# Performance work log

Measured on AMD Instinct MI355X. Metric: run time of the kernel, lower is better.

Reference implementation:

```python
import jax, jax.numpy as jnp
import numpy as np

BS, N, H = 8, 64, 512
L = 5
HH, WW = 14, 14


def setup_inputs() -> dict:
    key = jax.random.key(0)
    ks = jax.random.split(key, 6)
    roi_feature_single = jax.random.normal(ks[0], (BS, N, H), dtype=jnp.float32)
    img_featmap = jax.random.normal(ks[1], (BS, H, HH, WW), dtype=jnp.float32)
    # torch init: weight ~ N(0, 0.01), bias = 0
    node_W = jax.random.normal(ks[2], (L, H, H), dtype=jnp.float32) * 0.01
    node_b = jnp.zeros((L, H), dtype=jnp.float32)
    edge_W = jax.random.normal(ks[3], (L, H, H), dtype=jnp.float32) * 0.01
    edge_b = jnp.zeros((L, H), dtype=jnp.float32)
    full_mask = jax.random.randint(ks[4], (BS, N, N), 0, 2, dtype=jnp.int32)
    return {
        "roi_feature_single": roi_feature_single,
        "img_featmap": img_featmap,
        "node_W": node_W,
        "node_b": node_b,
        "edge_W": edge_W,
        "edge_b": edge_b,
        "full_mask": full_mask,
    }


def reference(roi_feature_single, img_featmap, node_W, node_b, edge_W, edge_b, full_mask):
    # mask: [bs, N, N, 1], float
    mask = full_mask.astype(jnp.float32)[..., None]
    denom = jnp.sum(mask, axis=-2) + 1.0  # [bs, N, 1]

    # AdaptiveAvgPool2d((1,1)) on N*N repeats of img_featmap == global mean over (H, W)
    edge_init = jnp.mean(img_featmap, axis=(2, 3))  # [bs, hidden]
    edge_state = jnp.broadcast_to(edge_init[:, None, None, :], (BS, N, N, H))

    node_state = roi_feature_single  # [bs, N, hidden]

    for t in range(L):
        nm = jnp.einsum('bnh,oh->bno', node_state, node_W[t]) + node_b[t]          # node_fc
        em = jnp.einsum('bijh,oh->bijo', edge_state, edge_W[t]) + edge_b[t]        # edge_fc
        col = nm[:, None, :, :]                      # feature_col_large [bs,1,N,h]
        edge_feat = nm[:, :, None, :] + col + em     # row + col + edge messages
        edge_state = jax.nn.leaky_relu(edge_feat)    # negative_slope=0.01 (torch default)
        agg = jnp.sum(edge_state * col * mask, axis=-2)   # masked sum over j -> [bs,N,h]
        node_feat = (nm + agg) / denom
        node_state = node_state + jax.nn.leaky_relu(node_feat)

    roi_col = jnp.broadcast_to(node_state[:, :, None, :], (BS, N, N, H))
    roi_row = jnp.broadcast_to(node_state[:, None, :, :], (BS, N, N, H))
    return jnp.concatenate([roi_col, roi_row], axis=-1)  # [bs, N, N, 2*hidden]
```

## Files before the change

### kernel.cpp

```cpp
#include <hip/hip_runtime.h>
#include <hip/hip_bf16.h>

#define BS 8
#define NN 64
#define HD 512
#define NLAYER 5

typedef short bf16x8 __attribute__((ext_vector_type(8)));
typedef float f32x4 __attribute__((ext_vector_type(4)));

__device__ __forceinline__ float lrelu(float x) { return x > 0.f ? x : 0.01f * x; }

__device__ __forceinline__ void cp16(const void* g, void* l) {
    __builtin_amdgcn_global_load_lds(
        (const __attribute__((address_space(1))) unsigned int*)g,
        (__attribute__((address_space(3))) unsigned int*)l,
        16, 0, 0);
}

__global__ __launch_bounds__(256) void prep_kernel(
    const float* __restrict__ roi, const float* __restrict__ img,
    const float* __restrict__ nW, const float* __restrict__ eW,
    const int* __restrict__ mask,
    __hip_bfloat16* __restrict__ nWb, __hip_bfloat16* __restrict__ eWb,
    float* __restrict__ nodef, __hip_bfloat16* __restrict__ nodeb,
    float* __restrict__ edge_init, float* __restrict__ denom)
{
    int bid = blockIdx.x, tid = threadIdx.x;
    if (bid < 2560) {
        const float* src = (bid < 1280) ? nW : eW;
        __hip_bfloat16* dst = (bid < 1280) ? nWb : eWb;
        int base = ((bid < 1280) ? bid : bid - 1280) * 1024 + tid * 4;
#pragma unroll
        for (int k = 0; k < 4; ++k) dst[base + k] = __float2bfloat16(src[base + k]);
    } else if (bid < 2816) {
        int base = (bid - 2560) * 1024 + tid * 4;
#pragma unroll
        for (int k = 0; k < 4; ++k) {
            float v = roi[base + k];
            nodef[base + k] = v;
            nodeb[base + k] = __float2bfloat16(v);
        }
    } else if (bid < 3840) {
        int pid = (bid - 2816) * 4 + (tid >> 6);
        int l = tid & 63;
        const float* p = img + (size_t)pid * 196;
        float s = 0.f;
        for (int x = l; x < 196; x += 64) s += p[x];
#pragma unroll
        for (int off = 1; off < 64; off <<= 1) s += __shfl_xor(s, off, 64);
        if (l == 0) edge_init[pid] = s * (1.f / 196.f);
    } else {
        int pid = (bid - 3840) * 256 + tid;
        if (pid < 512) {
            const int* m = mask + pid * 64;
            int s = 0;
#pragma unroll
            for (int j = 0; j < 64; ++j) s += m[j];
            denom[pid] = (float)s + 1.f;
        }
    }
}

__global__ __launch_bounds__(256) void em0_kernel(
    const float* __restrict__ edge_init,
    const float* __restrict__ eW0,
    const float* __restrict__ eB0,
    float* __restrict__ em0)
{
    int W = blockIdx.x * 4 + (threadIdx.x >> 6);
    int l = threadIdx.x & 63;
    int b = W >> 9, o = W & 511;
    const float4* ei = (const float4*)(edge_init + b * 512);
    const float4* w4 = (const float4*)(eW0 + (size_t)o * 512);
    float4 a0 = ei[l * 2], a1 = ei[l * 2 + 1];
    float4 b0 = w4[l * 2], b1 = w4[l * 2 + 1];
    float s = a0.x * b0.x + a0.y * b0.y + a0.z * b0.z + a0.w * b0.w
            + a1.x * b1.x + a1.y * b1.y + a1.z * b1.z + a1.w * b1.w;
#pragma unroll
    for (int off = 1; off < 64; off <<= 1) s += __shfl_xor(s, off, 64);
    if (l == 0) em0[W] = s + eB0[o];
}

__global__ __launch_bounds__(256, 4) void nm_gemm(
    const __hip_bfloat16* __restrict__ A,
    const __hip_bfloat16* __restrict__ W,
    const float* __restrict__ bias,
    float* __restrict__ nm)
{
    __shared__ __align__(16) __hip_bfloat16 sA[32 * 64];
    __shared__ __align__(16) __hip_bfloat16 sB[64 * 64];
    int tid = threadIdx.x;
    int bm = blockIdx.x, bn = blockIdx.y;
    int w = tid >> 6, l = tid & 63;
    int wm = w & 1, wn = w >> 1;
    int lq = l >> 4, lr = l & 15;

    const char* aBase = (const char*)A + (size_t)bm * 32 * 1024;
    const char* bBase = (const char*)W + (size_t)bn * 64 * 1024;
    int rowA = tid >> 3;
    int gA = rowA * 1024 + (((tid & 7) ^ (rowA & 7)) << 4);
    int lO = tid * 16;
    int sw = lr & 7;

    f32x4 acc[2] = {};

    for (int kt = 0; kt < 8; ++kt) {
        int ko = kt * 128;
        cp16(aBase + gA + ko, (char*)sA + lO);
        cp16(bBase + gA + ko, (char*)sB + lO);
        cp16(bBase + gA + 32768 + ko, (char*)sB + lO + 4096);
        __syncthreads();
#pragma unroll
        for (int kk = 0; kk < 2; ++kk) {
            bf16x8 af = *(const bf16x8*)&sA[(wm * 16 + lr) * 64 + (((kk * 4 + lq) ^ sw) << 3)];
#pragma unroll
            for (int ni = 0; ni < 2; ++ni) {
                bf16x8 bv = *(const bf16x8*)&sB[(wn * 32 + ni * 16 + lr) * 64 + (((kk * 4 + lq) ^ sw) << 3)];
                acc[ni] = __builtin_amdgcn_mfma_f32_16x16x32_bf16(af, bv, acc[ni], 0, 0, 0);
            }
        }
        __syncthreads();
    }
#pragma unroll
    for (int ni = 0; ni < 2; ++ni) {
        int col = bn * 64 + wn * 32 + ni * 16 + lr;
        float bv = bias[col];
#pragma unroll
        for (int r = 0; r < 4; ++r) {
            int row = bm * 32 + wm * 16 + lq * 4 + r;
            nm[(size_t)row * 512 + col] = acc[ni][r] + bv;
        }
    }
}

__global__ __launch_bounds__(256) void edge_rank1(
    const float* __restrict__ nm, const float* __restrict__ em0,
    const int* __restrict__ mask,
    __hip_bfloat16* __restrict__ es_dst,
    const float* __restrict__ denom,
    float* __restrict__ nodef, __hip_bfloat16* __restrict__ nodeb)
{
    int g = blockIdx.x >> 1, ch = blockIdx.x & 1;
    int w = threadIdx.x >> 6, l = threadIdx.x & 63;
    int c = ch * 256 + w * 64 + l;
    int b = g >> 6;
    float nmi = nm[(size_t)g * 512 + c];
    float emb = em0[b * 512 + c];
    const float* nmb = nm + (size_t)b * 64 * 512;
    const int* mrow = mask + g * 64;
    __hip_bfloat16* erow = es_dst + (size_t)g * 64 * 512 + c;
    float aggv = 0.f;
#pragma unroll 4
    for (int j = 0; j < 64; ++j) {
        float nmj = nmb[j * 512 + c];
        float es = lrelu(nmi + nmj + emb);
        erow[(size_t)j * 512] = __float2bfloat16(es);
        aggv += es * nmj * (float)mrow[j];
    }
    float nf = (nmi + aggv) / denom[g];
    size_t idx = (size_t)g * 512 + c;
    float ns = nodef[idx] + lrelu(nf);
    nodef[idx] = ns;
    nodeb[idx] = __float2bfloat16(ns);
}

__global__ __launch_bounds__(256, 4) void edge_fused(
    const __hip_bfloat16* __restrict__ es_src,
    const __hip_bfloat16* __restrict__ eW,
    const float* __restrict__ eB,
    const float* __restrict__ nm,
    const int* __restrict__ mask,
    __hip_bfloat16* __restrict__ es_dst,
    const float* __restrict__ denom,
    float* __restrict__ nodef, __hip_bfloat16* __restrict__ nodeb,
    int write_es)
{
    __shared__ __align__(16) __hip_bfloat16 sA[128 * 64];
    __shared__ __align__(16) __hip_bfloat16 sB[128 * 64];
    int tid = threadIdx.x;
    int lid = blockIdx.y * 4 + blockIdx.x;
    int xcd = lid & 7, idx = lid >> 3;
    int bm = xcd + ((idx >> 2) << 3);
    int bn = idx & 3;
    int w = tid >> 6, l = tid & 63;
    int wm = w >> 1, wn = w & 1;
    int lq = l >> 4, lr = l & 15;

    const char* aBase = (const char*)es_src + (size_t)bm * 128 * 1024;
    const char* bBase = (const char*)eW + (size_t)bn * 128 * 1024;
    int rrow = tid >> 3;
    int gOff = rrow * 1024 + ((((tid & 7) ^ (rrow & 7))) << 4);
    int lOff = tid * 16;
    int sw = lr & 7;

    f32x4 acc[4][4] = {};

    for (int kt = 0; kt < 8; ++kt) {
        int ko = kt * 128;
#pragma unroll
        for (int i = 0; i < 4; ++i) {
            cp16(aBase + gOff + i * 32768 + ko, (char*)sA + lOff + i * 4096);
            cp16(bBase + gOff + i * 32768 + ko, (char*)sB + lOff + i * 4096);
        }
        __syncthreads();
#pragma unroll
        for (int kk = 0; kk < 2; ++kk) {
            bf16x8 af[4], bfv[4];
#pragma unroll
            for (int mi = 0; mi < 4; ++mi)
                af[mi] = *(const bf16x8*)&sA[(wm * 64 + mi * 16 + lr) * 64 + (((kk * 4 + lq) ^ sw) << 3)];
#pragma unroll
            for (int ni = 0; ni < 4; ++ni)
                bfv[ni] = *(const bf16x8*)&sB[(wn * 64 + ni * 16 + lr) * 64 + (((kk * 4 + lq) ^ sw) << 3)];
#pragma unroll
            for (int mi = 0; mi < 4; ++mi)
#pragma unroll
                for (int ni = 0; ni < 4; ++ni)
                    acc[mi][ni] = __builtin_amdgcn_mfma_f32_16x16x32_bf16(af[mi], bfv[ni], acc[mi][ni], 0, 0, 0);
        }
        __syncthreads();
    }

    int g = bm * 2 + wm;
    int b = g >> 6;
    int cbase = bn * 128 + wn * 64;

    float nmraw[4], nmi[4];
#pragma unroll
    for (int ni = 0; ni < 4; ++ni) {
        int c = cbase + ni * 16 + lr;
        nmraw[ni] = nm[(size_t)g * 512 + c];
        nmi[ni] = nmraw[ni] + eB[c];
    }
    const float* nmb = nm + (size_t)b * 64 * 512;
    const int* mrow = mask + g * 64;
    float aggv[4] = {0.f, 0.f, 0.f, 0.f};

#pragma unroll
    for (int mi = 0; mi < 4; ++mi) {
#pragma unroll
        for (int r = 0; r < 4; ++r) {
            int j = mi * 16 + lq * 4 + r;
            float mf = (float)mrow[j];
            const float* nrow = nmb + (size_t)j * 512;
            size_t erow = ((size_t)(g * 64 + j)) * 512;
#pragma unroll
            for (int ni = 0; ni < 4; ++ni) {
                int c = cbase + ni * 16 + lr;
                float nmj = nrow[c];
                float es = lrelu(acc[mi][ni][r] + nmi[ni] + nmj);
                if (write_es) es_dst[erow + c] = __float2bfloat16(es);
                aggv[ni] += es * nmj * mf;
            }
        }
    }
    float dinv = denom[g];
#pragma unroll
    for (int ni = 0; ni < 4; ++ni) {
        float v = aggv[ni];
        v += __shfl_xor(v, 16, 64);
        v += __shfl_xor(v, 32, 64);
        if (lq == 0) {
            size_t oidx = (size_t)g * 512 + cbase + ni * 16 + lr;
            float nf = (nmraw[ni] + v) / dinv;
            float ns = nodef[oidx] + lrelu(nf);
            nodef[oidx] = ns;
            nodeb[oidx] = __float2bfloat16(ns);
        }
    }
}

__global__ __launch_bounds__(256) void out_kernel(
    const float* __restrict__ nodef, float* __restrict__ out)
{
    size_t ch = (size_t)blockIdx.x * 256 + threadIdx.x;
    int c4 = (int)(ch & 255);
    size_t r = ch >> 8;
    int b = (int)(r >> 12);
    int i = (int)((r >> 6) & 63);
    int j = (int)(r & 63);
    int c = c4 * 4;
    const float* src = (c < 512) ? (nodef + ((size_t)(b * 64 + i)) * 512 + c)
                                 : (nodef + ((size_t)(b * 64 + j)) * 512 + (c - 512));
    *reinterpret_cast<float4*>(out + ch * 4) = *reinterpret_cast<const float4*>(src);
}

extern "C" void kernel_launch(void* const* d_in, const int* in_sizes, int n_in,
                              void* d_out, int out_size, void* d_ws, size_t ws_size,
                              hipStream_t stream) {
    const float* roi  = (const float*)d_in[0];
    const float* img  = (const float*)d_in[1];
    const float* nW   = (const float*)d_in[2];
    const float* nB   = (const float*)d_in[3];
    const float* eW   = (const float*)d_in[4];
    const float* eB   = (const float*)d_in[5];
    const int*   mask = (const int*)d_in[6];

    char* ob = (char*)d_out;
    const size_t ES_BYTES = (size_t)32768 * 512 * 2;
    __hip_bfloat16* es0   = (__hip_bfloat16*)(ob);
    __hip_bfloat16* es1   = (__hip_bfloat16*)(ob + ES_BYTES);
    __hip_bfloat16* eWb   = (__hip_bfloat16*)(ob + 2 * ES_BYTES);
    __hip_bfloat16* nWb   = (__hip_bfloat16*)(ob + 2 * ES_BYTES + 2621440);
    __hip_bfloat16* nodeb = (__hip_bfloat16*)(ob + 2 * ES_BYTES + 5242880);
    float*          nm    = (float*)(ob + 2 * ES_BYTES + 5767168);
    float*       edge_init= (float*)(ob + 2 * ES_BYTES + 6815744);
    float*          em0   = (float*)(ob + 2 * ES_BYTES + 6832128);

    char* ws = (char*)d_ws;
    float* nodef = (float*)(ws);
    float* denom = (float*)(ws + 1048576);
    float* outp  = (float*)d_out;

    prep_kernel<<<3842, 256, 0, stream>>>(roi, img, nW, eW, mask,
                                          nWb, eWb, nodef, nodeb, edge_init, denom);
    em0_kernel<<<1024, 256, 0, stream>>>(edge_init, eW, eB, em0);

    nm_gemm<<<dim3(16, 8), 256, 0, stream>>>(nodeb, nWb, nB, nm);
    edge_rank1<<<1024, 256, 0, stream>>>(nm, em0, mask, es0, denom, nodef, nodeb);

    for (int t = 1; t < NLAYER; ++t) {
        const __hip_bfloat16* src = (t & 1) ? es0 : es1;
        __hip_bfloat16* dst       = (t & 1) ? es1 : es0;
        nm_gemm<<<dim3(16, 8), 256, 0, stream>>>(nodeb, nWb + (size_t)t * 262144,
                                                 nB + t * 512, nm);
        edge_fused<<<dim3(4, 256), 256, 0, stream>>>(src, eWb + (size_t)t * 262144,
                                                     eB + t * 512, nm, mask,
                                                     dst, denom, nodef, nodeb,
                                                     (t < 4) ? 1 : 0);
    }

    out_kernel<<<32768, 256, 0, stream>>>(nodef, outp);
}
```

Before: 400.8 us.

## Split fused edge GEMM+epilogue into separate em GEMM and elementwise epilogue kernels

Replaces the fused edge_fused kernel with two kernels: em_gemm, which keeps a full 64x512 weight slice resident in LDS and streams A rows directly from global into MFMA, writing a bf16 edge-message buffer; and edge_ep, a per-(g,c) elementwise epilogue that reads that buffer, applies leaky ReLU, writes the edge state and does the masked aggregation without shuffles. The intent is to simplify the GEMM inner loop (no per-k-tile LDS staging or barriers for A) and make the epilogue coalesced. The cost is an extra 32 MB intermediate round trip per layer through HBM/L2, an extra bf16 rounding of the edge messages, and one extra launch per layer.

```diff
diff --git a/kernel.cpp b/kernel.cpp
--- a/kernel.cpp
+++ b/kernel.cpp
@@ -142,8 +142,7 @@
     float* __restrict__ nodef, __hip_bfloat16* __restrict__ nodeb)
 {
     int g = blockIdx.x >> 1, ch = blockIdx.x & 1;
-    int w = threadIdx.x >> 6, l = threadIdx.x & 63;
-    int c = ch * 256 + w * 64 + l;
+    int c = ch * 256 + threadIdx.x;
     int b = g >> 6;
     float nmi = nm[(size_t)g * 512 + c];
     float emb = em0[b * 512 + c];
@@ -165,110 +164,90 @@
     nodeb[idx] = __float2bfloat16(ns);
 }
 
-__global__ __launch_bounds__(256, 4) void edge_fused(
+__global__ __launch_bounds__(256, 2) void em_gemm(
     const __hip_bfloat16* __restrict__ es_src,
     const __hip_bfloat16* __restrict__ eW,
+    __hip_bfloat16* __restrict__ em)
+{
+    __shared__ __align__(16) __hip_bfloat16 sB[64 * 512];
+    int tid = threadIdx.x;
+    int bn = blockIdx.x;
+    int bm = blockIdx.y;
+    int wv = tid >> 6, l = tid & 63;
+    int lq = l >> 4, lr = l & 15;
+
+    const char* bBase = (const char*)eW + (size_t)bn * 65536;
+#pragma unroll
+    for (int i = 0; i < 16; ++i) {
+        int chunk = tid + i * 256;
+        int srcOff = (chunk & ~63) * 16 + (((chunk & 63) ^ ((chunk >> 6) & 7)) << 4);
+        cp16(bBase + srcOff, (char*)sB + chunk * 16);
+    }
+    __syncthreads();
+
+    int rbase = bm * 128 + wv * 32;
+    const char* aBase = (const char*)es_src + (size_t)rbase * 1024;
+    const char* sBb = (const char*)sB;
+
+    f32x4 acc[2][4] = {};
+#pragma unroll
+    for (int kq = 0; kq < 16; ++kq) {
+        bf16x8 a0 = *(const bf16x8*)(aBase + lr * 1024 + kq * 64 + lq * 16);
+        bf16x8 a1 = *(const bf16x8*)(aBase + (16 + lr) * 1024 + kq * 64 + lq * 16);
+#pragma unroll
+        for (int cg = 0; cg < 4; ++cg) {
+            int rl = cg * 16 + lr;
+            bf16x8 bf = *(const bf16x8*)(sBb + rl * 1024 + ((((kq * 4 + lq) ^ (rl & 7))) << 4));
+            acc[0][cg] = __builtin_amdgcn_mfma_f32_16x16x32_bf16(a0, bf, acc[0][cg], 0, 0, 0);
+            acc[1][cg] = __builtin_amdgcn_mfma_f32_16x16x32_bf16(a1, bf, acc[1][cg], 0, 0, 0);
+        }
+    }
+
+#pragma unroll
+    for (int rg = 0; rg < 2; ++rg)
+#pragma unroll
+        for (int cg = 0; cg < 4; ++cg)
+#pragma unroll
+            for (int r = 0; r < 4; ++r) {
+                int row = rbase + rg * 16 + lq * 4 + r;
+                int col = bn * 64 + cg * 16 + lr;
+                em[(size_t)row * 512 + col] = __float2bfloat16(acc[rg][cg][r]);
+            }
+}
+
+__global__ __launch_bounds__(256) void edge_ep(
+    const __hip_bfloat16* __restrict__ em,
+    const float* __restrict__ nm,
     const float* __restrict__ eB,
-    const float* __restrict__ nm,
     const int* __restrict__ mask,
     __hip_bfloat16* __restrict__ es_dst,
     const float* __restrict__ denom,
     float* __restrict__ nodef, __hip_bfloat16* __restrict__ nodeb,
     int write_es)
 {
-    __shared__ __align__(16) __hip_bfloat16 sA[128 * 64];
-    __shared__ __align__(16) __hip_bfloat16 sB[128 * 64];
-    int tid = threadIdx.x;
-    int lid = blockIdx.y * 4 + blockIdx.x;
-    int xcd = lid & 7, idx = lid >> 3;
-    int bm = xcd + ((idx >> 2) << 3);
-    int bn = idx & 3;
-    int w = tid >> 6, l = tid & 63;
-    int wm = w >> 1, wn = w & 1;
-    int lq = l >> 4, lr = l & 15;
-
-    const char* aBase = (const char*)es_src + (size_t)bm * 128 * 1024;
-    const char* bBase = (const char*)eW + (size_t)bn * 128 * 1024;
-    int rrow = tid >> 3;
-    int gOff = rrow * 1024 + ((((tid & 7) ^ (rrow & 7))) << 4);
-    int lOff = tid * 16;
-    int sw = lr & 7;
-
-    f32x4 acc[4][4] = {};
-
-    for (int kt = 0; kt < 8; ++kt) {
-        int ko = kt * 128;
-#pragma unroll
-        for (int i = 0; i < 4; ++i) {
-            cp16(aBase + gOff + i * 32768 + ko, (char*)sA + lOff + i * 4096);
-            cp16(bBase + gOff + i * 32768 + ko, (char*)sB + lOff + i * 4096);
-        }
-        __syncthreads();
-#pragma unroll
-        for (int kk = 0; kk < 2; ++kk) {
-            bf16x8 af[4], bfv[4];
-#pragma unroll
-            for (int mi = 0; mi < 4; ++mi)
-                af[mi] = *(const bf16x8*)&sA[(wm * 64 + mi * 16 + lr) * 64 + (((kk * 4 + lq) ^ sw) << 3)];
-#pragma unroll
-            for (int ni = 0; ni < 4; ++ni)
-                bfv[ni] = *(const bf16x8*)&sB[(wn * 64 + ni * 16 + lr) * 64 + (((kk * 4 + lq) ^ sw) << 3)];
-#pragma unroll
-            for (int mi = 0; mi < 4; ++mi)
-#pragma unroll
-                for (int ni = 0; ni < 4; ++ni)
-                    acc[mi][ni] = __builtin_amdgcn_mfma_f32_16x16x32_bf16(af[mi], bfv[ni], acc[mi][ni], 0, 0, 0);
-        }
-        __syncthreads();
-    }
-
-    int g = bm * 2 + wm;
+    int g = blockIdx.x >> 1, ch = blockIdx.x & 1;
+    int c = ch * 256 + threadIdx.x;
     int b = g >> 6;
-    int cbase = bn * 128 + wn * 64;
-
-    float nmraw[4], nmi[4];
-#pragma unroll
-    for (int ni = 0; ni < 4; ++ni) {
-        int c = cbase + ni * 16 + lr;
-        nmraw[ni] = nm[(size_t)g * 512 + c];
-        nmi[ni] = nmraw[ni] + eB[c];
-    }
+    float nmraw = nm[(size_t)g * 512 + c];
+    float nmi = nmraw + eB[c];
+    const __hip_bfloat16* emrow = em + (size_t)g * 64 * 512 + c;
     const float* nmb = nm + (size_t)b * 64 * 512;
     const int* mrow = mask + g * 64;
-    float aggv[4] = {0.f, 0.f, 0.f, 0.f};
-
-#pragma unroll
-    for (int mi = 0; mi < 4; ++mi) {
-#pragma unroll
-        for (int r = 0; r < 4; ++r) {
-            int j = mi * 16 + lq * 4 + r;
-            float mf = (float)mrow[j];
-            const float* nrow = nmb + (size_t)j * 512;
-            size_t erow = ((size_t)(g * 64 + j)) * 512;
-#pragma unroll
-            for (int ni = 0; ni < 4; ++ni) {
-                int c = cbase + ni * 16 + lr;
-                float nmj = nrow[c];
-                float es = lrelu(acc[mi][ni][r] + nmi[ni] + nmj);
-                if (write_es) es_dst[erow + c] = __float2bfloat16(es);
-                aggv[ni] += es * nmj * mf;
-            }
-        }
-    }
-    float dinv = denom[g];
-#pragma unroll
-    for (int ni = 0; ni < 4; ++ni) {
-        float v = aggv[ni];
-        v += __shfl_xor(v, 16, 64);
-        v += __shfl_xor(v, 32, 64);
-        if (lq == 0) {
-            size_t oidx = (size_t)g * 512 + cbase + ni * 16 + lr;
-            float nf = (nmraw[ni] + v) / dinv;
-            float ns = nodef[oidx] + lrelu(nf);
-            nodef[oidx] = ns;
-            nodeb[oidx] = __float2bfloat16(ns);
-        }
-    }
+    __hip_bfloat16* erow = es_dst + (size_t)g * 64 * 512 + c;
+    float aggv = 0.f;
+#pragma unroll 4
+    for (int j = 0; j < 64; ++j) {
+        float emv = __bfloat162float(emrow[(size_t)j * 512]);
+        float nmj = nmb[j * 512 + c];
+        float es = lrelu(emv + nmi + nmj);
+        if (write_es) erow[(size_t)j * 512] = __float2bfloat16(es);
+        aggv += es * nmj * (float)mrow[j];
+    }
+    float nf = (nmraw + aggv) / denom[g];
+    size_t idx = (size_t)g * 512 + c;
+    float ns = nodef[idx] + lrelu(nf);
+    nodef[idx] = ns;
+    nodeb[idx] = __float2bfloat16(ns);
 }
 
 __global__ __launch_bounds__(256) void out_kernel(
@@ -301,12 +280,13 @@
     const size_t ES_BYTES = (size_t)32768 * 512 * 2;
     __hip_bfloat16* es0   = (__hip_bfloat16*)(ob);
     __hip_bfloat16* es1   = (__hip_bfloat16*)(ob + ES_BYTES);
-    __hip_bfloat16* eWb   = (__hip_bfloat16*)(ob + 2 * ES_BYTES);
-    __hip_bfloat16* nWb   = (__hip_bfloat16*)(ob + 2 * ES_BYTES + 2621440);
-    __hip_bfloat16* nodeb = (__hip_bfloat16*)(ob + 2 * ES_BYTES + 5242880);
-    float*          nm    = (float*)(ob + 2 * ES_BYTES + 5767168);
-    float*       edge_init= (float*)(ob + 2 * ES_BYTES + 6815744);
-    float*          em0   = (float*)(ob + 2 * ES_BYTES + 6832128);
+    __hip_bfloat16* emb   = (__hip_bfloat16*)(ob + 2 * ES_BYTES);
+    __hip_bfloat16* eWb   = (__hip_bfloat16*)(ob + 3 * ES_BYTES);
+    __hip_bfloat16* nWb   = (__hip_bfloat16*)(ob + 3 * ES_BYTES + 2621440);
+    __hip_bfloat16* nodeb = (__hip_bfloat16*)(ob + 3 * ES_BYTES + 5242880);
+    float*          nm    = (float*)(ob + 3 * ES_BYTES + 5767168);
+    float*       edge_init= (float*)(ob + 3 * ES_BYTES + 6815744);
+    float*          em0   = (float*)(ob + 3 * ES_BYTES + 6832128);
 
     char* ws = (char*)d_ws;
     float* nodef = (float*)(ws);
@@ -325,10 +305,10 @@
         __hip_bfloat16* dst       = (t & 1) ? es1 : es0;
         nm_gemm<<<dim3(16, 8), 256, 0, stream>>>(nodeb, nWb + (size_t)t * 262144,
                                                  nB + t * 512, nm);
-        edge_fused<<<dim3(4, 256), 256, 0, stream>>>(src, eWb + (size_t)t * 262144,
-                                                     eB + t * 512, nm, mask,
-                                                     dst, denom, nodef, nodeb,
-                                                     (t < 4) ? 1 : 0);
+        em_gemm<<<dim3(8, 256), 256, 0, stream>>>(src, eWb + (size_t)t * 262144, emb);
+        edge_ep<<<1024, 256, 0, stream>>>(emb, nm, eB + t * 512, mask,
+                                          dst, denom, nodef, nodeb,
+                                          (t < 4) ? 1 : 0);
     }
 
     out_kernel<<<32768, 256, 0, stream>>>(nodef, outp);
```

Result: slower. 504.4 us (+25.8%).

## Shrink edge GEMM tiles to 64x64 per block and drop XCD swizzle

Applied to the files above, without the earlier changes.

The fused edge GEMM+epilogue kernel now computes a 64x64 output tile per block instead of 128x128. Each wave owns a 16-column strip across all 64 rows, with a single B fragment reused against four A fragments. The grid grows from 1024 to 4096 blocks and the launch bound is raised to 6 blocks per CU, aiming for more parallelism and occupancy with fewer accumulator registers. In exchange each block reloads more A/B data relative to its MFMA work, so arithmetic intensity drops and global/LDS traffic rises, and the XCD-aware block remapping is removed. A small indexing simplification in edge_rank1 is also included.

```diff
diff --git a/kernel.cpp b/kernel.cpp
--- a/kernel.cpp
+++ b/kernel.cpp
@@ -142,8 +142,7 @@
     float* __restrict__ nodef, __hip_bfloat16* __restrict__ nodeb)
 {
     int g = blockIdx.x >> 1, ch = blockIdx.x & 1;
-    int w = threadIdx.x >> 6, l = threadIdx.x & 63;
-    int c = ch * 256 + w * 64 + l;
+    int c = ch * 256 + threadIdx.x;
     int b = g >> 6;
     float nmi = nm[(size_t)g * 512 + c];
     float emb = em0[b * 512 + c];
@@ -165,7 +164,7 @@
     nodeb[idx] = __float2bfloat16(ns);
 }
 
-__global__ __launch_bounds__(256, 4) void edge_fused(
+__global__ __launch_bounds__(256, 6) void edge_fused(
     const __hip_bfloat16* __restrict__ es_src,
     const __hip_bfloat16* __restrict__ eW,
     const float* __restrict__ eB,
@@ -176,66 +175,51 @@
     float* __restrict__ nodef, __hip_bfloat16* __restrict__ nodeb,
     int write_es)
 {
-    __shared__ __align__(16) __hip_bfloat16 sA[128 * 64];
-    __shared__ __align__(16) __hip_bfloat16 sB[128 * 64];
+    __shared__ __align__(16) __hip_bfloat16 sA[64 * 64];
+    __shared__ __align__(16) __hip_bfloat16 sB[64 * 64];
     int tid = threadIdx.x;
-    int lid = blockIdx.y * 4 + blockIdx.x;
-    int xcd = lid & 7, idx = lid >> 3;
-    int bm = xcd + ((idx >> 2) << 3);
-    int bn = idx & 3;
+    int bm = blockIdx.x;
+    int bn = blockIdx.y;
     int w = tid >> 6, l = tid & 63;
-    int wm = w >> 1, wn = w & 1;
     int lq = l >> 4, lr = l & 15;
 
-    const char* aBase = (const char*)es_src + (size_t)bm * 128 * 1024;
-    const char* bBase = (const char*)eW + (size_t)bn * 128 * 1024;
+    const char* aBase = (const char*)es_src + (size_t)bm * 64 * 1024;
+    const char* bBase = (const char*)eW + (size_t)bn * 64 * 1024;
     int rrow = tid >> 3;
     int gOff = rrow * 1024 + ((((tid & 7) ^ (rrow & 7))) << 4);
     int lOff = tid * 16;
     int sw = lr & 7;
 
-    f32x4 acc[4][4] = {};
+    f32x4 acc[4] = {};
 
     for (int kt = 0; kt < 8; ++kt) {
         int ko = kt * 128;
-#pragma unroll
-        for (int i = 0; i < 4; ++i) {
-            cp16(aBase + gOff + i * 32768 + ko, (char*)sA + lOff + i * 4096);
-            cp16(bBase + gOff + i * 32768 + ko, (char*)sB + lOff + i * 4096);
-        }
+        cp16(aBase + gOff + ko,         (char*)sA + lOff);
+        cp16(aBase + gOff + 32768 + ko, (char*)sA + lOff + 4096);
+        cp16(bBase + gOff + ko,         (char*)sB + lOff);
+        cp16(bBase + gOff + 32768 + ko, (char*)sB + lOff + 4096);
         __syncthreads();
 #pragma unroll
         for (int kk = 0; kk < 2; ++kk) {
-            bf16x8 af[4], bfv[4];
-#pragma unroll
-            for (int mi = 0; mi < 4; ++mi)
-                af[mi] = *(const bf16x8*)&sA[(wm * 64 + mi * 16 + lr) * 64 + (((kk * 4 + lq) ^ sw) << 3)];
-#pragma unroll
-            for (int ni = 0; ni < 4; ++ni)
-                bfv[ni] = *(const bf16x8*)&sB[(wn * 64 + ni * 16 + lr) * 64 + (((kk * 4 + lq) ^ sw) << 3)];
-#pragma unroll
-            for (int mi = 0; mi < 4; ++mi)
-#pragma unroll
-                for (int ni = 0; ni < 4; ++ni)
-                    acc[mi][ni] = __builtin_amdgcn_mfma_f32_16x16x32_bf16(af[mi], bfv[ni], acc[mi][ni], 0, 0, 0);
+            bf16x8 bf = *(const bf16x8*)&sB[(w * 16 + lr) * 64 + (((kk * 4 + lq) ^ sw) << 3)];
+#pragma unroll
+            for (int mi = 0; mi < 4; ++mi) {
+                bf16x8 af = *(const bf16x8*)&sA[(mi * 16 + lr) * 64 + (((kk * 4 + lq) ^ sw) << 3)];
+                acc[mi] = __builtin_amdgcn_mfma_f32_16x16x32_bf16(af, bf, acc[mi], 0, 0, 0);
+            }
         }
         __syncthreads();
     }
 
-    int g = bm * 2 + wm;
+    int g = bm;
     int b = g >> 6;
-    int cbase = bn * 128 + wn * 64;
-
-    float nmraw[4], nmi[4];
-#pragma unroll
-    for (int ni = 0; ni < 4; ++ni) {
-        int c = cbase + ni * 16 + lr;
-        nmraw[ni] = nm[(size_t)g * 512 + c];
-        nmi[ni] = nmraw[ni] + eB[c];
-    }
+    int c = bn * 64 + w * 16 + lr;
+
+    float nmraw = nm[(size_t)g * 512 + c];
+    float nmi = nmraw + eB[c];
     const float* nmb = nm + (size_t)b * 64 * 512;
     const int* mrow = mask + g * 64;
-    float aggv[4] = {0.f, 0.f, 0.f, 0.f};
+    float aggv = 0.f;
 
 #pragma unroll
     for (int mi = 0; mi < 4; ++mi) {
@@ -243,31 +227,20 @@
         for (int r = 0; r < 4; ++r) {
             int j = mi * 16 + lq * 4 + r;
             float mf = (float)mrow[j];
-            const float* nrow = nmb + (size_t)j * 512;
-            size_t erow = ((size_t)(g * 64 + j)) * 512;
-#pragma unroll
-            for (int ni = 0; ni < 4; ++ni) {
-                int c = cbase + ni * 16 + lr;
-                float nmj = nrow[c];
-                float es = lrelu(acc[mi][ni][r] + nmi[ni] + nmj);
-                if (write_es) es_dst[erow + c] = __float2bfloat16(es);
-                aggv[ni] += es * nmj * mf;
-            }
-        }
-    }
-    float dinv = denom[g];
-#pragma unroll
-    for (int ni = 0; ni < 4; ++ni) {
-        float v = aggv[ni];
-        v += __shfl_xor(v, 16, 64);
-        v += __shfl_xor(v, 32, 64);
-        if (lq == 0) {
-            size_t oidx = (size_t)g * 512 + cbase + ni * 16 + lr;
-            float nf = (nmraw[ni] + v) / dinv;
-            float ns = nodef[oidx] + lrelu(nf);
-            nodef[oidx] = ns;
-            nodeb[oidx] = __float2bfloat16(ns);
-        }
+            float nmj = nmb[(size_t)j * 512 + c];
+            float es = lrelu(acc[mi][r] + nmi + nmj);
+            if (write_es) es_dst[((size_t)(g * 64 + j)) * 512 + c] = __float2bfloat16(es);
+            aggv += es * nmj * mf;
+        }
+    }
+    aggv += __shfl_xor(aggv, 16, 64);
+    aggv += __shfl_xor(aggv, 32, 64);
+    if (lq == 0) {
+        size_t oidx = (size_t)g * 512 + c;
+        float nf = (nmraw + aggv) / denom[g];
+        float ns = nodef[oidx] + lrelu(nf);
+        nodef[oidx] = ns;
+        nodeb[oidx] = __float2bfloat16(ns);
     }
 }
 
@@ -325,7 +298,7 @@
         __hip_bfloat16* dst       = (t & 1) ? es1 : es0;
         nm_gemm<<<dim3(16, 8), 256, 0, stream>>>(nodeb, nWb + (size_t)t * 262144,
                                                  nB + t * 512, nm);
-        edge_fused<<<dim3(4, 256), 256, 0, stream>>>(src, eWb + (size_t)t * 262144,
+        edge_fused<<<dim3(512, 8), 256, 0, stream>>>(src, eWb + (size_t)t * 262144,
                                                      eB + t * 512, nm, mask,
                                                      dst, denom, nodef, nodeb,
                                                      (t < 4) ? 1 : 0);
```

Result: faster. 361.1 us (-9.9%).
